# Kernel optimization log

Measured on AMD Instinct MI355X. Metric: run time of the kernel, lower is better.

## Reference

```python
import jax, jax.numpy as jnp
import numpy as np

B, S, DM, H = 2, 2048, 1024, 16
HD = DM // H
SCALE = 1.0 / np.sqrt(HD)  # temperature = 1.0
LN_EPS = 1e-5


def setup_inputs() -> dict:
    key = jax.random.key(0)
    ks = jax.random.split(key, 12)
    s = 1.0 / np.sqrt(DM)
    inp = {
        'x': jax.random.normal(ks[0], (B, S, DM), dtype=jnp.float32),
        'Wq': jax.random.uniform(ks[1], (DM, DM), jnp.float32, -s, s),
        'bq': jnp.zeros((DM,), jnp.float32),
        'Wk': jax.random.uniform(ks[2], (DM, DM), jnp.float32, -s, s),
        'bk': jnp.zeros((DM,), jnp.float32),
        'Wv': jax.random.uniform(ks[3], (DM, DM), jnp.float32, -s, s),
        'bv': jnp.zeros((DM,), jnp.float32),
        'Wo': jax.random.uniform(ks[4], (DM, DM), jnp.float32, -s, s),
        'bo': jnp.zeros((DM,), jnp.float32),
        'Wg': jax.random.uniform(ks[5], (DM, DM), jnp.float32, -s, s),
        'bg': jnp.zeros((DM,), jnp.float32),
        'attention_weights': jnp.ones((H,), jnp.float32),
        'ln_gamma': jnp.ones((DM,), jnp.float32),
        'ln_beta': jnp.zeros((DM,), jnp.float32),
    }
    return inp


def _forward(x, Wq, bq, Wk, bk, Wv, bv, Wo, bo, Wg, bg, attention_weights, ln_gamma, ln_beta):
    # projections -> [B, H, S, HD]
    def split_heads(t):
        return t.reshape(B, S, H, HD).transpose(0, 2, 1, 3)
    q = split_heads(x @ Wq.T + bq)
    k = split_heads(x @ Wk.T + bk)
    v = split_heads(x @ Wv.T + bv)
    # scores [B, H, S, S]; no softmax: exact-erf GELU activation instead
    scores = jnp.einsum('bhsd,bhtd->bhst', q, k) * SCALE
    attn = jax.nn.gelu(scores, approximate=False)
    head_w = jax.nn.softmax(attention_weights)  # [H]
    attn = attn * head_w[None, :, None, None]
    # context [B, S, DM]
    ctx = jnp.einsum('bhst,bhtd->bhsd', attn, v).transpose(0, 2, 1, 3).reshape(B, S, DM)
    out = ctx @ Wo.T + bo
    gate = jax.nn.sigmoid(out @ Wg.T + bg)
    out = gate * out + (1.0 - gate) * x
    y = out + x
    mu = jnp.mean(y, axis=-1, keepdims=True)
    var = jnp.var(y, axis=-1, keepdims=True)
    return (y - mu) / jnp.sqrt(var + LN_EPS) * ln_gamma + ln_beta


def reference(x, Wq, bq, Wk, bk, Wv, bv, Wo, bo, Wg, bg, attention_weights, ln_gamma, ln_beta):
    return _forward(x, Wq, bq, Wk, bk, Wv, bv, Wo, bo, Wg, bg, attention_weights, ln_gamma, ln_beta)
```

## Files before the change

kernel.cpp:

```cpp
#include <hip/hip_runtime.h>
#include <hip/hip_bf16.h>

#define B_ 2
#define S_ 2048
#define DM_ 1024
#define H_ 16
#define HD_ 64
#define QKVLD 3072
#define WELT_ ((size_t)DM_ * DM_)

using bf16x8 = __attribute__((ext_vector_type(8))) short;
using f16x2  = __attribute__((ext_vector_type(2))) _Float16;
using f16x8  = __attribute__((ext_vector_type(8))) _Float16;
using f32x4  = __attribute__((ext_vector_type(4))) float;
using f32x16 = __attribute__((ext_vector_type(16))) float;

#define GLOAD16(g, l) __builtin_amdgcn_global_load_lds( \
    (const __attribute__((address_space(1))) void*)(g), \
    (__attribute__((address_space(3))) void*)(l), 16, 0, 0)

__device__ __forceinline__ int swz128(int row, int bytecol) {
    return row * 128 + (bytecol ^ ((row & 7) << 4));
}

__device__ __forceinline__ ushort bf16_rne(float f) {
    uint b = __builtin_bit_cast(uint, f);
    b += 0x7FFF + ((b >> 16) & 1);
    return (ushort)(b >> 16);
}

__device__ __forceinline__ float bf16_to_f(ushort u) {
    return __builtin_bit_cast(float, (uint)u << 16);
}

__device__ __forceinline__ void pl32swap(uint& a, uint& b) {
    asm volatile("v_permlane32_swap_b32 %0, %1" : "+v"(a), "+v"(b));
}

__device__ __forceinline__ f16x2 cvt_pk_f16(float lo, float hi) {
    return __builtin_bit_cast(f16x2, __builtin_amdgcn_cvt_pkrtz(lo, hi));
}

__device__ __forceinline__ f16x2 gelu_h2(f16x2 x) {
    const f16x2 C3 = {(_Float16)-0.00074855f, (_Float16)-0.00074855f};
    const f16x2 C2 = {(_Float16)0.0146724f,   (_Float16)0.0146724f};
    const f16x2 C1 = {(_Float16)-0.1266945f,  (_Float16)-0.1266945f};
    const f16x2 C0 = {(_Float16)0.7966101f,   (_Float16)0.7966101f};
    const f16x2 ONE = {(_Float16)1.0f, (_Float16)1.0f};
    const f16x2 NEG = {(_Float16)-1.0f, (_Float16)-1.0f};
    const f16x2 HLF = {(_Float16)0.5f, (_Float16)0.5f};
    f16x2 u = x * x;
    f16x2 t = C3 * u + C2;
    t = t * u + C1;
    t = t * u + C0;
    f16x2 e = x * t;
    e = __builtin_elementwise_min(__builtin_elementwise_max(e, NEG), ONE);
    f16x2 hx = x * HLF;
    return hx * e + hx;
}

__global__ __launch_bounds__(256) void prep_kernel(
    const float* __restrict__ x, __hip_bfloat16* __restrict__ xb,
    const float* __restrict__ Wq, const float* __restrict__ Wk, const float* __restrict__ Wv,
    const float* __restrict__ Wo, const float* __restrict__ Wg,
    const float* __restrict__ bq, const float* __restrict__ bk, const float* __restrict__ bv,
    const float* __restrict__ bo, const float* __restrict__ bg,
    const float* __restrict__ aw, __hip_bfloat16* __restrict__ Wall,
    __hip_bfloat16* __restrict__ Wcomb, __hip_bfloat16* __restrict__ Wot,
    float* __restrict__ bqkv, float* __restrict__ bcomb)
{
    __shared__ ushort stile[64][72];
    auto headw = [&](int h) {
        float mx = aw[0];
        for (int i = 1; i < H_; ++i) mx = fmaxf(mx, aw[i]);
        float sm = 0.f;
        for (int i = 0; i < H_; ++i) sm += expf(aw[i] - mx);
        return expf(aw[h] - mx) / sm;
    };
    const int tid = threadIdx.x;
    int blk = blockIdx.x;
    if (blk < 4096) {
        int i = blk * 1024 + tid * 4;
        float4 v = *(const float4*)(x + i);
        ushort4 o = { bf16_rne(v.x), bf16_rne(v.y), bf16_rne(v.z), bf16_rne(v.w) };
        *(ushort4*)(xb + i) = o;
    } else if (blk < 9216) {
        blk -= 4096;
        int widx = blk >> 10;
        int row = blk & 1023;
        int off = row * 1024 + tid * 4;
        const float* src = widx == 0 ? Wq : widx == 1 ? Wk : widx == 2 ? Wv : widx == 3 ? Wo : Wg;
        float scale = widx == 0 ? 0.125f : 1.0f;
        if (widx == 2) scale = headw(row >> 6);
        __hip_bfloat16* dst = (widx == 3) ? Wcomb
                            : Wall + (size_t)(widx == 4 ? 3 : widx) * WELT_;
        float4 v = *(const float4*)(src + off);
        ushort4 o = { bf16_rne(v.x * scale), bf16_rne(v.y * scale),
                      bf16_rne(v.z * scale), bf16_rne(v.w * scale) };
        *(ushort4*)(dst + off) = o;
    } else if (blk < 9228) {
        int i = (blk - 9216) * 256 + tid;
        if (i < 3 * DM_) {
            float v;
            if (i < DM_) v = bq[i] * 0.125f;
            else if (i < 2 * DM_) v = bk[i - DM_];
            else v = bv[i - 2 * DM_] * headw((i - 2 * DM_) >> 6);
            bqkv[i] = v;
        }
    } else if (blk < 9484) {
        int idx = blk - 9228;
        const int c0 = (idx & 15) * 64, r0 = (idx >> 4) * 64;
#pragma unroll
        for (int c = tid; c < 1024; c += 256) {
            int row = c >> 4, cg = c & 15;
            float4 v = *(const float4*)(Wo + (size_t)(r0 + row) * 1024 + c0 + cg * 4);
            stile[row][cg * 4 + 0] = bf16_rne(v.x);
            stile[row][cg * 4 + 1] = bf16_rne(v.y);
            stile[row][cg * 4 + 2] = bf16_rne(v.z);
            stile[row][cg * 4 + 3] = bf16_rne(v.w);
        }
        __syncthreads();
#pragma unroll
        for (int c = tid; c < 512; c += 256) {
            int d = c >> 3, tg = c & 7;
            union { ushort u[8]; float4 v; } tmp;
#pragma unroll
            for (int j = 0; j < 8; ++j) tmp.u[j] = stile[tg * 8 + j][d];
            *(float4*)(Wot + (size_t)(c0 + d) * 1024 + r0 + tg * 8) = tmp.v;
        }
    } else {
        int idx = blk - 9484;
        const int w = tid >> 6, lane = tid & 63;
        if (idx < 4) bcomb[idx * 256 + tid] = bo[idx * 256 + tid];
        const int row = idx * 4 + w;
        float s = 0.f;
        for (int k = lane; k < 1024; k += 64) s += Wg[row * 1024 + k] * bo[k];
#pragma unroll
        for (int off = 32; off > 0; off >>= 1) s += __shfl_down(s, off, 64);
        if (lane == 0) bcomb[1024 + row] = bg[row] + s;
    }
}

__global__ __launch_bounds__(256, 4) void gemm_nt_kernel(
    const __hip_bfloat16* __restrict__ A, int lda,
    const __hip_bfloat16* __restrict__ Bw, int ldb,
    const float* __restrict__ bias, float* __restrict__ Cf,
    __hip_bfloat16* __restrict__ Cb, int ldc, int K, int gx1, int nblk1,
    const __hip_bfloat16* __restrict__ A2, const __hip_bfloat16* __restrict__ B2,
    __hip_bfloat16* __restrict__ C2, _Float16* __restrict__ Vt2, int nblk_tot)
{
    __shared__ __align__(16) char smem[32768];
    const int tid = threadIdx.x;
    const int w = tid >> 6, lane = tid & 63, hi = lane >> 4, lo = lane & 15;
    const int wr = w >> 1, wc = w & 1;

    int bid = blockIdx.x;
    bid = (bid & 7) * (nblk_tot >> 3) + (bid >> 3);

    const __hip_bfloat16 *Ap, *Bp;
    const float* bp;
    float* cf;
    __hip_bfloat16* cb;
    int LDA, LDB, LDC, KK, bx, by;
    if (bid < nblk1) {
        bx = bid % gx1; by = bid / gx1;
        Ap = A; Bp = Bw; bp = bias; cf = Cf; cb = Cb;
        LDA = lda; LDB = ldb; LDC = ldc; KK = K;
    } else {
        int t2 = bid - nblk1;
        bx = t2 & 7; by = t2 >> 3;
        Ap = A2; Bp = B2; bp = nullptr; cf = nullptr; cb = C2;
        LDA = DM_; LDB = DM_; LDC = DM_; KK = DM_;
    }
    const int m0 = by * 128, n0 = bx * 128;

    const int srow = lane >> 3;
    const int scol = (lane & 7) ^ srow;
    const __hip_bfloat16* sbase;
    int sld;
    char* lbase;
    if (w < 2) {
        sbase = Ap + (size_t)(m0 + w * 64 + srow) * LDA + scol * 8;
        sld = LDA;
        lbase = smem + w * 8192;
    } else {
        sbase = Bp + (size_t)(n0 + (w - 2) * 64 + srow) * LDB + scol * 8;
        sld = LDB;
        lbase = smem + 16384 + (w - 2) * 8192;
    }

    f32x4 acc[4][4];
#pragma unroll
    for (int m = 0; m < 4; ++m)
#pragma unroll
        for (int n = 0; n < 4; ++n) acc[m][n] = (f32x4){0.f, 0.f, 0.f, 0.f};

    for (int k0 = 0; k0 < KK; k0 += 64) {
#pragma unroll
        for (int i = 0; i < 8; ++i)
            GLOAD16(sbase + (size_t)i * 8 * sld + k0, lbase + i * 1024);
        __syncthreads();
#pragma unroll
        for (int ks = 0; ks < 2; ++ks) {
            bf16x8 af[4], bfr[4];
#pragma unroll
            for (int m = 0; m < 4; ++m)
                af[m] = *(const bf16x8*)(smem + swz128(wr * 64 + m * 16 + lo, ks * 64 + hi * 16));
#pragma unroll
            for (int n = 0; n < 4; ++n)
                bfr[n] = *(const bf16x8*)(smem + 16384 + swz128(wc * 64 + n * 16 + lo, ks * 64 + hi * 16));
#pragma unroll
            for (int m = 0; m < 4; ++m)
#pragma unroll
                for (int n = 0; n < 4; ++n)
                    acc[m][n] = __builtin_amdgcn_mfma_f32_16x16x32_bf16(af[m], bfr[n], acc[m][n], 0, 0, 0);
        }
        __syncthreads();
    }

    if (Vt2 && bid < nblk1 && bx >= 16) {
        ushort* vtile = (ushort*)smem;
        const int bq = m0 >> 11;
        const int trow0 = m0 - bq * 2048;
#pragma unroll
        for (int n = 0; n < 4; ++n) {
            int gcl = wc * 64 + n * 16 + lo;
            float bz = bp[n0 + gcl];
            int s = (gcl & 7) << 3;
#pragma unroll
            for (int m = 0; m < 4; ++m) {
                int grl = wr * 64 + m * 16 + hi * 4;
                f16x2 p0 = cvt_pk_f16(acc[m][n][0] + bz, acc[m][n][1] + bz);
                f16x2 p1 = cvt_pk_f16(acc[m][n][2] + bz, acc[m][n][3] + bz);
                ushort* dst = vtile + gcl * 128 + (grl ^ s);
                *(uint*)(dst)     = __builtin_bit_cast(uint, p0);
                *(uint*)(dst + 2) = __builtin_bit_cast(uint, p1);
            }
        }
        __syncthreads();
        const int dg0 = n0 - 2048;
#pragma unroll
        for (int i = 0; i < 8; ++i) {
            int idx = i * 256 + tid;
            int dl = idx >> 4, tg = idx & 15;
            int s = (dl & 7) << 3;
            float4 v = *(const float4*)(vtile + dl * 128 + ((tg * 8) ^ s));
            int dglob = dg0 + dl;
            int h = dglob >> 6, d = dglob & 63;
            *(float4*)(Vt2 + ((size_t)((bq * H_ + h) * HD_) + d) * S_ + trow0 + tg * 8) = v;
        }
        return;
    }

#pragma unroll
    for (int n = 0; n < 4; ++n) {
        int gc = n0 + wc * 64 + n * 16 + lo;
        float bz = bp ? bp[gc] : 0.f;
#pragma unroll
        for (int m = 0; m < 4; ++m) {
            int gr = m0 + wr * 64 + m * 16 + hi * 4;
#pragma unroll
            for (int r = 0; r < 4; ++r) {
                float v = acc[m][n][r] + bz;
                size_t o = (size_t)(gr + r) * LDC + gc;
                if (cf) cf[o] = v;
                if (cb) *(ushort*)(cb + o) = bf16_rne(v);
            }
        }
    }
}

__global__ __launch_bounds__(512) void attn_kernel(
    const __hip_bfloat16* __restrict__ QKV, const _Float16* __restrict__ Vt,
    __hip_bfloat16* __restrict__ ctx)
{
    __shared__ __align__(16) char lds[2][16384];

    const int tid = threadIdx.x;
    const int w = tid >> 6, lane = tid & 63;
    const int l31 = lane & 31, hi2 = lane >> 5;
    const int qg = w & 3, th = w >> 2;
    const int nq = S_ / 128;
    int blk = blockIdx.x;
    blk = (blk & 7) * 64 + (blk >> 3);
    const int q0 = (blk % nq) * 128;
    const int bh = blk / nq;
    const int h = bh % H_, b = bh / H_;

    bf16x8 qf[4];
    {
        const __hip_bfloat16* qrow = QKV + ((size_t)(b * S_ + q0 + qg * 32 + l31) * QKVLD + h * HD_);
#pragma unroll
        for (int ks = 0; ks < 4; ++ks)
            qf[ks] = *(const bf16x8*)(qrow + ks * 16 + hi2 * 8);
    }

    const bool isK = (w < 4);
    const int f0 = (isK ? w : (w - 4)) * 2;
    const char* sp[2];
    int loff[2];
#pragma unroll
    for (int j = 0; j < 2; ++j) {
        int f = f0 + j;
        if (isK) {
            sp[j] = (const char*)(QKV + (size_t)(b * S_ + (f >> 2) * 32 + l31) * QKVLD + DM_ + h * HD_ + (f & 3) * 16 + hi2 * 8);
            loff[j] = f * 1024;
        } else {
            sp[j] = (const char*)(Vt + ((size_t)((b * H_ + h) * HD_) + (f >> 2) * 32 + l31) * S_ + (f & 3) * 16 + hi2 * 8);
            loff[j] = 8192 + f * 1024;
        }
    }
    const size_t tstep = isK ? (size_t)128 * QKVLD : (size_t)128;

#define STAGE(buf) do { \
    _Pragma("unroll") \
    for (int j = 0; j < 2; ++j) { \
        GLOAD16(sp[j], lds[buf] + loff[j]); \
        sp[j] += tstep; \
    } } while (0)

    f32x16 cacc[2];
#pragma unroll
    for (int n = 0; n < 2; ++n)
#pragma unroll
        for (int r = 0; r < 16; ++r) cacc[n][r] = 0.f;

    STAGE(0);
    asm volatile("s_waitcnt vmcnt(0)" ::: "memory");
    __builtin_amdgcn_s_barrier();

    const int lane16 = lane * 16;
    const int NT = S_ / 64;
    for (int t = 0; t < NT; ++t) {
        const int cur = t & 1;
        if (t + 1 < NT) STAGE(cur ^ 1);

        __builtin_amdgcn_s_setprio(1);
        f32x16 sacc;
#pragma unroll
        for (int r = 0; r < 16; ++r) sacc[r] = 0.f;
#pragma unroll
        for (int ks = 0; ks < 4; ++ks) {
            bf16x8 kf = *(const bf16x8*)(lds[cur] + (th * 4 + ks) * 1024 + lane16);
            sacc = __builtin_amdgcn_mfma_f32_32x32x16_bf16(kf, qf[ks], sacc, 0, 0, 0);
        }
        f16x2 P[8];
#pragma unroll
        for (int i = 0; i < 8; ++i)
            P[i] = gelu_h2(cvt_pk_f16(sacc[2 * i], sacc[2 * i + 1]));
        uint a0 = __builtin_bit_cast(uint, P[0]), b0 = __builtin_bit_cast(uint, P[2]);
        uint a1 = __builtin_bit_cast(uint, P[1]), b1 = __builtin_bit_cast(uint, P[3]);
        uint a2 = __builtin_bit_cast(uint, P[4]), b2 = __builtin_bit_cast(uint, P[6]);
        uint a3 = __builtin_bit_cast(uint, P[5]), b3 = __builtin_bit_cast(uint, P[7]);
        pl32swap(a0, b0); pl32swap(a1, b1); pl32swap(a2, b2); pl32swap(a3, b3);
        union { uint u[4]; f16x8 v; } pa0, pa1;
        pa0.u[0] = a0; pa0.u[1] = a1; pa0.u[2] = b0; pa0.u[3] = b1;
        pa1.u[0] = a2; pa1.u[1] = a3; pa1.u[2] = b2; pa1.u[3] = b3;
#pragma unroll
        for (int kc2 = 0; kc2 < 2; ++kc2) {
            int kc = th * 2 + kc2;
            f16x8 pa = kc2 ? pa1.v : pa0.v;
#pragma unroll
            for (int n2 = 0; n2 < 2; ++n2) {
                f16x8 vf = *(const f16x8*)(lds[cur] + 8192 + (n2 * 4 + kc) * 1024 + lane16);
                cacc[n2] = __builtin_amdgcn_mfma_f32_32x32x16_f16(pa, vf, cacc[n2], 0, 0, 0);
            }
        }
        __builtin_amdgcn_s_setprio(0);
        asm volatile("s_waitcnt vmcnt(0)" ::: "memory");
        __builtin_amdgcn_s_barrier();
    }

    char* red = (char*)lds;
    if (th == 1) {
#pragma unroll
        for (int n2 = 0; n2 < 2; ++n2)
#pragma unroll
            for (int r = 0; r < 16; ++r)
                *(float*)(red + qg * 8192 + (n2 * 16 + r) * 256 + lane * 4) = cacc[n2][r];
    }
    __syncthreads();
    if (th == 0) {
#pragma unroll
        for (int n2 = 0; n2 < 2; ++n2)
#pragma unroll
            for (int r = 0; r < 16; ++r) {
                float v = cacc[n2][r] +
                    *(const float*)(red + qg * 8192 + (n2 * 16 + r) * 256 + lane * 4);
                int qrow = (r & 3) + 8 * (r >> 2) + 4 * hi2;
                size_t o = (size_t)(b * S_ + q0 + qg * 32 + qrow) * DM_ + h * HD_ + n2 * 32 + l31;
                *(ushort*)(ctx + o) = bf16_rne(v);
            }
    }
#undef STAGE
}

__global__ __launch_bounds__(256) void epilogue_ln_kernel(
    const __hip_bfloat16* __restrict__ og, const __hip_bfloat16* __restrict__ xb,
    const float* __restrict__ gamma, const float* __restrict__ beta,
    float* __restrict__ y)
{
    const int row = blockIdx.x, tid = threadIdx.x;
    const size_t obase = (size_t)row * 2048 + tid * 4;
    const size_t xbase = (size_t)row * DM_ + tid * 4;
    ushort4 ob = *(const ushort4*)(og + obase);
    ushort4 gb = *(const ushort4*)(og + obase + 1024);
    ushort4 xv = *(const ushort4*)(xb + xbase);
    float yv[4];
    float s = 0.f, s2 = 0.f;
    const ushort* obp = (const ushort*)&ob;
    const ushort* gbp = (const ushort*)&gb;
    const ushort* xp  = (const ushort*)&xv;
#pragma unroll
    for (int j = 0; j < 4; ++j) {
        float o = bf16_to_f(obp[j]), g = bf16_to_f(gbp[j]), xx = bf16_to_f(xp[j]);
        float gate = __builtin_amdgcn_rcpf(1.f + __expf(-g));
        float yy = gate * o + (1.f - gate) * xx + xx;
        yv[j] = yy;
        s += yy; s2 += yy * yy;
    }
    const int w = tid >> 6, lane = tid & 63;
#pragma unroll
    for (int off = 32; off > 0; off >>= 1) {
        s  += __shfl_down(s, off, 64);
        s2 += __shfl_down(s2, off, 64);
    }
    __shared__ float red[8];
    if (lane == 0) { red[w] = s; red[4 + w] = s2; }
    __syncthreads();
    s  = red[0] + red[1] + red[2] + red[3];
    s2 = red[4] + red[5] + red[6] + red[7];
    const float mu = s * (1.f / DM_);
    const float var = s2 * (1.f / DM_) - mu * mu;
    const float rstd = rsqrtf(var + 1e-5f);
    float4 outv;
#pragma unroll
    for (int j = 0; j < 4; ++j) {
        int col = tid * 4 + j;
        ((float*)&outv)[j] = (yv[j] - mu) * rstd * gamma[col] + beta[col];
    }
    *(float4*)(y + xbase) = outv;
}

extern "C" void kernel_launch(void* const* d_in, const int* in_sizes, int n_in,
                              void* d_out, int out_size, void* d_ws, size_t ws_size,
                              hipStream_t stream) {
    const float* x  = (const float*)d_in[0];
    const float* Wq = (const float*)d_in[1];
    const float* bq = (const float*)d_in[2];
    const float* Wk = (const float*)d_in[3];
    const float* bk = (const float*)d_in[4];
    const float* Wv = (const float*)d_in[5];
    const float* bv = (const float*)d_in[6];
    const float* Wo = (const float*)d_in[7];
    const float* bo = (const float*)d_in[8];
    const float* Wg = (const float*)d_in[9];
    const float* bg = (const float*)d_in[10];
    const float* aw = (const float*)d_in[11];
    const float* gamma = (const float*)d_in[12];
    const float* beta  = (const float*)d_in[13];

    char* ws = (char*)d_ws;
    size_t off = 0;
    auto alloc = [&](size_t bytes) -> char* {
        char* p = ws + off;
        off += (bytes + 255) & ~(size_t)255;
        return p;
    };
    const size_t NTOK = (size_t)B_ * S_;
    const size_t NELT = NTOK * DM_;

    __hip_bfloat16* xb    = (__hip_bfloat16*)alloc(NELT * 2);
    __hip_bfloat16* Wall  = (__hip_bfloat16*)alloc(4 * WELT_ * 2);
    __hip_bfloat16* Wot   = (__hip_bfloat16*)alloc(WELT_ * 2);
    __hip_bfloat16* Wcomb = (__hip_bfloat16*)alloc(2 * WELT_ * 2);
    float*          bqkv  = (float*)alloc(3 * DM_ * 4);
    float*          bcomb = (float*)alloc(2 * DM_ * 4);
    __hip_bfloat16* qkvb  = (__hip_bfloat16*)alloc(NTOK * QKVLD * 2);
    _Float16*       Vtb   = (_Float16*)alloc(NELT * 2);
    __hip_bfloat16* ctxb  = (__hip_bfloat16*)alloc(NELT * 2);
    __hip_bfloat16* ogb   = (__hip_bfloat16*)alloc(NTOK * 2048 * 2);

    prep_kernel<<<9740, 256, 0, stream>>>(x, xb, Wq, Wk, Wv, Wo, Wg,
                                          bq, bk, bv, bo, bg, aw,
                                          Wall, Wcomb, Wot, bqkv, bcomb);

    gemm_nt_kernel<<<768 + 64, 256, 0, stream>>>(
        xb, DM_, Wall, DM_, bqkv, nullptr, qkvb, QKVLD, DM_, 24, 768,
        Wall + 3 * WELT_, Wot, Wcomb + WELT_, Vtb, 832);

    attn_kernel<<<B_ * H_ * (S_ / 128), 512, 0, stream>>>(qkvb, Vtb, ctxb);

    gemm_nt_kernel<<<512, 256, 0, stream>>>(
        ctxb, DM_, Wcomb, DM_, bcomb, nullptr, ogb, 2048, DM_, 16, 1 << 30,
        nullptr, nullptr, nullptr, nullptr, 512);

    epilogue_ln_kernel<<<(int)NTOK, 256, 0, stream>>>(ogb, xb, gamma, beta, (float*)d_out);
}
```

Baseline: 136.8 us.

## Triple-buffer attention K/V tiles and software-pipeline QK with GELU-PV

Moves the attention kernel from double to triple LDS buffering. Each iteration issues the QK^T MFMAs for the next tile before the GELU and PV work of the current tile, so the matrix and elementwise units can interleave, and it waits with vmcnt(2) so one global load stays in flight. This adds 16KB of LDS per block, which may lower occupancy, and it makes the buffer rotation and barrier logic more complex.

```diff
diff --git a/kernel.cpp b/kernel.cpp
--- a/kernel.cpp
+++ b/kernel.cpp
@@ -274,7 +274,7 @@
     const __hip_bfloat16* __restrict__ QKV, const _Float16* __restrict__ Vt,
     __hip_bfloat16* __restrict__ ctx)
 {
-    __shared__ __align__(16) char lds[2][16384];
+    __shared__ __align__(16) char lds[3][16384];
 
     const int tid = threadIdx.x;
     const int w = tid >> 6, lane = tid & 63;
@@ -312,10 +312,10 @@
     }
     const size_t tstep = isK ? (size_t)128 * QKVLD : (size_t)128;
 
-#define STAGE(buf) do { \
+#define STAGE(bufp) do { \
     _Pragma("unroll") \
     for (int j = 0; j < 2; ++j) { \
-        GLOAD16(sp[j], lds[buf] + loff[j]); \
+        GLOAD16(sp[j], (bufp) + loff[j]); \
         sp[j] += tstep; \
     } } while (0)
 
@@ -325,25 +325,20 @@
 #pragma unroll
         for (int r = 0; r < 16; ++r) cacc[n][r] = 0.f;
 
-    STAGE(0);
-    asm volatile("s_waitcnt vmcnt(0)" ::: "memory");
-    __builtin_amdgcn_s_barrier();
-
     const int lane16 = lane * 16;
-    const int NT = S_ / 64;
-    for (int t = 0; t < NT; ++t) {
-        const int cur = t & 1;
-        if (t + 1 < NT) STAGE(cur ^ 1);
-
-        __builtin_amdgcn_s_setprio(1);
-        f32x16 sacc;
-#pragma unroll
-        for (int r = 0; r < 16; ++r) sacc[r] = 0.f;
+
+    auto QK = [&](const char* base) {
+        f32x16 s;
+#pragma unroll
+        for (int r = 0; r < 16; ++r) s[r] = 0.f;
 #pragma unroll
         for (int ks = 0; ks < 4; ++ks) {
-            bf16x8 kf = *(const bf16x8*)(lds[cur] + (th * 4 + ks) * 1024 + lane16);
-            sacc = __builtin_amdgcn_mfma_f32_32x32x16_bf16(kf, qf[ks], sacc, 0, 0, 0);
-        }
+            bf16x8 kf = *(const bf16x8*)(base + (th * 4 + ks) * 1024 + lane16);
+            s = __builtin_amdgcn_mfma_f32_32x32x16_bf16(kf, qf[ks], s, 0, 0, 0);
+        }
+        return s;
+    };
+    auto GELUPV = [&](const f32x16& sacc, const char* base) {
         f16x2 P[8];
 #pragma unroll
         for (int i = 0; i < 8; ++i)
@@ -362,15 +357,53 @@
             f16x8 pa = kc2 ? pa1.v : pa0.v;
 #pragma unroll
             for (int n2 = 0; n2 < 2; ++n2) {
-                f16x8 vf = *(const f16x8*)(lds[cur] + 8192 + (n2 * 4 + kc) * 1024 + lane16);
+                f16x8 vf = *(const f16x8*)(base + 8192 + (n2 * 4 + kc) * 1024 + lane16);
                 cacc[n2] = __builtin_amdgcn_mfma_f32_32x32x16_f16(pa, vf, cacc[n2], 0, 0, 0);
             }
         }
+    };
+
+    const int NT = S_ / 64;
+
+    STAGE(lds[0]);
+    STAGE(lds[1]);
+    asm volatile("s_waitcnt vmcnt(2)" ::: "memory");
+    __builtin_amdgcn_s_barrier();
+    f32x16 sA = QK(lds[0]);
+    f32x16 sB;
+
+    const char *c0 = lds[0], *c1 = lds[1], *c2 = lds[2];
+    for (int t = 0; t < NT; t += 2) {
+        __builtin_amdgcn_s_barrier();
+        if (t + 2 < NT) {
+            STAGE((char*)c2);
+            asm volatile("s_waitcnt vmcnt(2)" ::: "memory");
+        } else {
+            asm volatile("s_waitcnt vmcnt(0)" ::: "memory");
+        }
+        __builtin_amdgcn_s_setprio(1);
+        sB = QK(c1);
+        GELUPV(sA, c0);
         __builtin_amdgcn_s_setprio(0);
-        asm volatile("s_waitcnt vmcnt(0)" ::: "memory");
+
         __builtin_amdgcn_s_barrier();
-    }
-
+        if (t + 3 < NT) {
+            STAGE((char*)c0);
+            asm volatile("s_waitcnt vmcnt(2)" ::: "memory");
+        } else {
+            asm volatile("s_waitcnt vmcnt(0)" ::: "memory");
+        }
+        __builtin_amdgcn_s_setprio(1);
+        if (t + 2 < NT) sA = QK(c2);
+        GELUPV(sB, c1);
+        __builtin_amdgcn_s_setprio(0);
+
+        const char* t0p = c0;
+        const char* t1p = c1;
+        c0 = c2; c1 = t0p; c2 = t1p;
+    }
+
+    __syncthreads();
     char* red = (char*)lds;
     if (th == 1) {
 #pragma unroll
```

Measured after the change: 137.7 us. Within noise of the previous version (+0.6%).
